# Performance work log

Measured on AMD Instinct MI355X. Metric: run time of the kernel, lower is better.

The kernel has to match this reference:

```python
import jax, jax.numpy as jnp
import numpy as np

NUM_HEADS = 8
WINDOW = 128  # num_previous_frames
EPS = 1e-5


def setup_inputs() -> dict:
    key = jax.random.key(0)
    ks = jax.random.split(key, 5)
    B, T, E = 8, 1024, 512
    x = jax.random.normal(ks[0], (B, T, E), dtype=jnp.float32)
    x_lengths = jax.random.randint(ks[1], (B,), 1, T + 1).astype(jnp.int32)
    gamma = jnp.ones((E,), dtype=jnp.float32)
    beta = jnp.zeros((E,), dtype=jnp.float32)
    sc_in = 1.0 / np.sqrt(E)
    w_in = jax.random.normal(ks[2], (3 * E, E), dtype=jnp.float32) * sc_in
    b_in = jnp.zeros((3 * E,), dtype=jnp.float32)
    w_out = jax.random.normal(ks[3], (E, E), dtype=jnp.float32) * sc_in
    b_out = jnp.zeros((E,), dtype=jnp.float32)
    return {"x": x, "x_lengths": x_lengths, "gamma": gamma, "beta": beta,
            "w_in": w_in, "b_in": b_in, "w_out": w_out, "b_out": b_out}


def _forward(x, gamma, beta, w_in, b_in, w_out, b_out):
    B, T, E = x.shape
    H = NUM_HEADS
    D = E // H
    # Timewise LayerNorm: normalize over channel dim per (batch, time)
    mu = jnp.mean(x, axis=-1, keepdims=True)
    var = jnp.mean(jnp.square(x - mu), axis=-1, keepdims=True)
    xn = (x - mu) * jax.lax.rsqrt(var + EPS) * gamma + beta
    # in-projection: qkv packed
    qkv = xn @ w_in.T + b_in  # [B,T,3E]
    q, k, v = jnp.split(qkv, 3, axis=-1)
    q = q.reshape(B, T, H, D)
    k = k.reshape(B, T, H, D)
    v = v.reshape(B, T, H, D)
    scale = 1.0 / np.sqrt(D)
    scores = jnp.einsum('bqhd,bkhd->bhqk', q * scale, k)  # [B,H,T,T]
    # banded causal mask: allow j in [i-WINDOW, i]
    i = jnp.arange(T)[:, None]
    j = jnp.arange(T)[None, :]
    allowed = (j <= i) & (j >= i - WINDOW)
    scores = jnp.where(allowed[None, None], scores, -jnp.inf)
    attn = jax.nn.softmax(scores, axis=-1)
    ctx = jnp.einsum('bhqk,bkhd->bqhd', attn, v).reshape(B, T, E)
    out = ctx @ w_out.T + b_out
    return out  # dropout is identity in eval mode


def reference(x, x_lengths, gamma, beta, w_in, b_in, w_out, b_out):
    del x_lengths  # unused by the original forward (no key_padding_mask passed)
    return _forward(x, gamma, beta, w_in, b_in, w_out, b_out)
```

## Files before the change

### kernel.cpp

```cpp
#include <hip/hip_runtime.h>
#include <stdint.h>

typedef __bf16 bf16;
typedef __bf16 bf16x4 __attribute__((ext_vector_type(4)));
typedef __bf16 bf16x8 __attribute__((ext_vector_type(8)));
typedef float f32x4 __attribute__((ext_vector_type(4)));

#define MFMA_16x16x32(a, b, c) __builtin_amdgcn_mfma_f32_16x16x32_bf16((a), (b), (c), 0, 0, 0)

__device__ __forceinline__ void gl_lds16(const bf16* g, bf16* l) {
    __builtin_amdgcn_global_load_lds(
        (const __attribute__((address_space(1))) void*)g,
        (__attribute__((address_space(3))) void*)l, 16, 0, 0);
}

__global__ __launch_bounds__(256) void prep_kernel(const float* __restrict__ x,
                                                   const float* __restrict__ gamma,
                                                   const float* __restrict__ beta,
                                                   const float* __restrict__ w_in,
                                                   const float* __restrict__ w_out,
                                                   bf16* __restrict__ xn,
                                                   bf16* __restrict__ cw_in,
                                                   bf16* __restrict__ cw_out) {
    const int bid = blockIdx.x;
    if (bid < 2048) {
        const int lane = threadIdx.x & 63;
        const int row = (bid << 2) + (threadIdx.x >> 6);
        const size_t base = (size_t)row * 512 + lane * 8;
        const float* xf = x + base;
        float4 a = *(const float4*)xf;
        float4 b = *(const float4*)(xf + 4);
        float f[8] = {a.x, a.y, a.z, a.w, b.x, b.y, b.z, b.w};
        float s = 0.f;
#pragma unroll
        for (int j = 0; j < 8; ++j) s += f[j];
#pragma unroll
        for (int off = 32; off >= 1; off >>= 1) s += __shfl_xor(s, off, 64);
        const float mu = s * (1.0f / 512.0f);
        float vs = 0.f;
#pragma unroll
        for (int j = 0; j < 8; ++j) { float d = f[j] - mu; vs += d * d; }
#pragma unroll
        for (int off = 32; off >= 1; off >>= 1) vs += __shfl_xor(vs, off, 64);
        const float rstd = rsqrtf(vs * (1.0f / 512.0f) + 1e-5f);
        float4 g0 = *(const float4*)(gamma + lane * 8);
        float4 g1 = *(const float4*)(gamma + lane * 8 + 4);
        float4 b0 = *(const float4*)(beta + lane * 8);
        float4 b1 = *(const float4*)(beta + lane * 8 + 4);
        float gg[8] = {g0.x, g0.y, g0.z, g0.w, g1.x, g1.y, g1.z, g1.w};
        float bb[8] = {b0.x, b0.y, b0.z, b0.w, b1.x, b1.y, b1.z, b1.w};
        bf16x8 o;
#pragma unroll
        for (int j = 0; j < 8; ++j)
            o[j] = (bf16)((f[j] - mu) * rstd * gg[j] + bb[j]);
        *(bf16x8*)(xn + base) = o;
    } else {
        const float* src;
        bf16* dst;
        int base;
        if (bid < 2432) { src = w_in;  dst = cw_in;  base = (bid - 2048) * 2048; }
        else            { src = w_out; dst = cw_out; base = (bid - 2432) * 2048; }
        const int i = base + threadIdx.x * 8;
        float4 a = *(const float4*)(src + i);
        float4 b = *(const float4*)(src + i + 4);
        float f[8] = {a.x, a.y, a.z, a.w, b.x, b.y, b.z, b.w};
        bf16x8 o;
#pragma unroll
        for (int j = 0; j < 8; ++j) o[j] = (bf16)f[j];
        *(bf16x8*)(dst + i) = o;
    }
}

template <int TM, typename OT>
__global__ __launch_bounds__(256) void gemm_bt(const bf16* __restrict__ A,
                                               const bf16* __restrict__ B,
                                               const float* __restrict__ bias,
                                               OT* __restrict__ C,
                                               int N, int K) {
    constexpr int MI = TM / 32;
    constexpr int NCA = TM * 8;
    __shared__ alignas(16) bf16 As[TM * 64];
    __shared__ alignas(16) bf16 Bs[128 * 64];
    const int tid = threadIdx.x;
    const int lane = tid & 63;
    const int wid = tid >> 6;
    const int wm = (wid >> 1) * (TM / 2), wn = (wid & 1) * 64;
    const int m0 = blockIdx.y * TM, n0 = blockIdx.x * 128;
    const int l15 = lane & 15, l16 = lane >> 4;

    f32x4 acc[MI][4] = {};

    const bf16* Abase = A + (size_t)m0 * K;
    const bf16* Bbase = B + (size_t)n0 * K;

    for (int k0 = 0; k0 < K; k0 += 64) {
#pragma unroll
        for (int c = tid; c < NCA; c += 256) {
            const int p = c / (TM * 4);
            const int r = (c % (TM * 4)) >> 2;
            const int ko = (c & 3) * 8 + p * 32;
            gl_lds16(Abase + (size_t)r * K + k0 + ko, &As[c * 8]);
        }
#pragma unroll
        for (int c = tid; c < 1024; c += 256) {
            const int p = c >> 9;
            const int r = (c & 511) >> 2;
            const int ko = (c & 3) * 8 + p * 32;
            gl_lds16(Bbase + (size_t)r * K + k0 + ko, &Bs[c * 8]);
        }
        __syncthreads();
#pragma unroll
        for (int h = 0; h < 2; ++h) {
            bf16x8 af[MI], bfr[4];
#pragma unroll
            for (int t = 0; t < MI; ++t)
                af[t] = *(const bf16x8*)&As[h * (TM * 32) + (wm + t * 16 + l15) * 32 + l16 * 8];
#pragma unroll
            for (int t = 0; t < 4; ++t)
                bfr[t] = *(const bf16x8*)&Bs[h * 4096 + (wn + t * 16 + l15) * 32 + l16 * 8];
#pragma unroll
            for (int i = 0; i < MI; ++i)
#pragma unroll
                for (int j = 0; j < 4; ++j)
                    acc[i][j] = MFMA_16x16x32(bfr[j], af[i], acc[i][j]);
        }
        __syncthreads();
    }

#pragma unroll
    for (int j = 0; j < 4; ++j) {
        const int colb = n0 + wn + j * 16 + (l16 << 2);
        const float4 bv = *(const float4*)(bias + colb);
#pragma unroll
        for (int i = 0; i < MI; ++i) {
            const int row = m0 + wm + i * 16 + l15;
            if constexpr (sizeof(OT) == 2) {
                bf16x4 o;
                o[0] = (bf16)(acc[i][j][0] + bv.x);
                o[1] = (bf16)(acc[i][j][1] + bv.y);
                o[2] = (bf16)(acc[i][j][2] + bv.z);
                o[3] = (bf16)(acc[i][j][3] + bv.w);
                *(bf16x4*)&C[(size_t)row * N + colb] = o;
            } else {
                float4 o;
                o.x = acc[i][j][0] + bv.x;
                o.y = acc[i][j][1] + bv.y;
                o.z = acc[i][j][2] + bv.z;
                o.w = acc[i][j][3] + bv.w;
                *(float4*)&C[(size_t)row * N + colb] = o;
            }
        }
    }
}

#define KS_STRIDE 72
#define VN_STRIDE 74
#define PW_STRIDE 72

__global__ __launch_bounds__(256) void attn_kernel(const bf16* __restrict__ qkv,
                                                   bf16* __restrict__ ctx) {
    __shared__ alignas(16) bf16 Ks[192 * KS_STRIDE];
    __shared__ alignas(16) bf16 Vn[192 * VN_STRIDE];
    __shared__ alignas(16) bf16 Pbuf[4 * 16 * PW_STRIDE];

    const int tid = threadIdx.x;
    const int lane = tid & 63, wid = tid >> 6;
    const int l15 = lane & 15, l16 = lane >> 4;
    const int bh = blockIdx.y, b = bh >> 3, h = bh & 7;
    const int q0 = blockIdx.x * 64;
    const int kv0 = (q0 > 128) ? (q0 - 128) : 0;
    const int nk = q0 + 64 - kv0;
    const size_t tokbase = (size_t)b * 1024;

    for (int c = tid; c < nk * 8; c += 256) {
        const int kk = c >> 3, dc = (c & 7) * 8;
        const bf16* src = qkv + (tokbase + kv0 + kk) * 1536 + h * 64 + dc;
        uint4 kw = *(const uint4*)(src + 512);
        *(uint4*)&Ks[kk * KS_STRIDE + dc] = kw;
        uint4 vw = *(const uint4*)(src + 1024);
        uint* vdst = (uint*)&Vn[kk * VN_STRIDE + dc];
        vdst[0] = vw.x; vdst[1] = vw.y; vdst[2] = vw.z; vdst[3] = vw.w;
    }

    const int qt0 = q0 + wid * 16;
    const bf16* qptr = qkv + (tokbase + qt0 + l15) * 1536 + h * 64;
    bf16x8 qa0 = *(const bf16x8*)(qptr + l16 * 8);
    bf16x8 qa1 = *(const bf16x8*)(qptr + 32 + l16 * 8);

    __syncthreads();

    bf16* Pw = &Pbuf[wid * 16 * PW_STRIDE];
    f32x4 of[4] = {};
    float mst[4], lst[4];
#pragma unroll
    for (int r = 0; r < 4; ++r) { mst[r] = -1e30f; lst[r] = 0.f; }

    const int ktstart = ((qt0 > 128) ? (qt0 - 128) : 0) & ~63;
    for (int kt = ktstart; kt <= qt0 + 15; kt += 64) {
        const int krel = kt - kv0;
        int kgn = ((qt0 + 15 - kt) >> 4) + 1;
        if (kgn > 4) kgn = 4;
        const int dlo = qt0 - 128 - kt;
        const int kglo = (dlo > 0) ? (dlo >> 4) : 0;

        f32x4 s[4] = {};
        __builtin_amdgcn_s_setprio(1);
#pragma unroll
        for (int kg = 0; kg < 4; ++kg) {
            if (kg >= kglo && kg < kgn) {
                const bf16* kb = &Ks[(krel + kg * 16 + l15) * KS_STRIDE + l16 * 8];
                s[kg] = MFMA_16x16x32(qa0, *(const bf16x8*)kb, s[kg]);
                s[kg] = MFMA_16x16x32(qa1, *(const bf16x8*)(kb + 32), s[kg]);
            }
        }
        __builtin_amdgcn_s_setprio(0);

#pragma unroll
        for (int r = 0; r < 4; ++r) {
            const int qa = qt0 + l16 * 4 + r;
            float v[4];
#pragma unroll
            for (int kg = 0; kg < 4; ++kg) {
                const int key = kt + kg * 16 + l15;
                const bool ok = (key <= qa) && (key >= qa - 128);
                v[kg] = ok ? s[kg][r] * 0.125f : -1e30f;
            }
            float mx = fmaxf(fmaxf(v[0], v[1]), fmaxf(v[2], v[3]));
#pragma unroll
            for (int off = 1; off < 16; off <<= 1)
                mx = fmaxf(mx, __shfl_xor(mx, off, 64));
            const float mnew = fmaxf(mst[r], mx);
            const float alpha = __expf(mst[r] - mnew);
            const float e0 = __expf(v[0] - mnew);
            const float e1 = __expf(v[1] - mnew);
            const float e2 = __expf(v[2] - mnew);
            const float e3 = __expf(v[3] - mnew);
            float rs = (e0 + e1) + (e2 + e3);
#pragma unroll
            for (int off = 1; off < 16; off <<= 1)
                rs += __shfl_xor(rs, off, 64);
            lst[r] = lst[r] * alpha + rs;
            mst[r] = mnew;
#pragma unroll
            for (int nt = 0; nt < 4; ++nt) of[nt][r] *= alpha;
            const int q = l16 * 4 + r;
            Pw[q * PW_STRIDE + l15] = (bf16)e0;
            Pw[q * PW_STRIDE + 16 + l15] = (bf16)e1;
            Pw[q * PW_STRIDE + 32 + l15] = (bf16)e2;
            Pw[q * PW_STRIDE + 48 + l15] = (bf16)e3;
        }
        __asm__ volatile("s_waitcnt lgkmcnt(0)" ::: "memory");

        const bool haveA = (kglo < 2);
        const bool haveB = (kgn > 2);
        __builtin_amdgcn_s_setprio(1);
        if (haveA) {
            bf16x8 pa = *(const bf16x8*)&Pw[l15 * PW_STRIDE + l16 * 8];
            int row[8];
#pragma unroll
            for (int j = 0; j < 8; ++j) {
                int rr = krel + l16 * 8 + j;
                row[j] = (rr < nk) ? rr : (nk - 1);
            }
#pragma unroll
            for (int nt = 0; nt < 4; ++nt) {
                bf16x8 vb;
#pragma unroll
                for (int j = 0; j < 8; ++j)
                    vb[j] = Vn[row[j] * VN_STRIDE + nt * 16 + l15];
                of[nt] = MFMA_16x16x32(pa, vb, of[nt]);
            }
        }
        if (haveB) {
            bf16x8 pa = *(const bf16x8*)&Pw[l15 * PW_STRIDE + 32 + l16 * 8];
            int row[8];
#pragma unroll
            for (int j = 0; j < 8; ++j) {
                int rr = krel + 32 + l16 * 8 + j;
                row[j] = (rr < nk) ? rr : (nk - 1);
            }
#pragma unroll
            for (int nt = 0; nt < 4; ++nt) {
                bf16x8 vb;
#pragma unroll
                for (int j = 0; j < 8; ++j)
                    vb[j] = Vn[row[j] * VN_STRIDE + nt * 16 + l15];
                of[nt] = MFMA_16x16x32(pa, vb, of[nt]);
            }
        }
        __builtin_amdgcn_s_setprio(0);
        __asm__ volatile("s_waitcnt lgkmcnt(0)" ::: "memory");
    }

    float linv[4];
#pragma unroll
    for (int r = 0; r < 4; ++r) linv[r] = 1.0f / lst[r];
    bf16* cbase = ctx + (tokbase + qt0) * 512 + h * 64;
#pragma unroll
    for (int nt = 0; nt < 4; ++nt)
#pragma unroll
        for (int r = 0; r < 4; ++r) {
            const int q = l16 * 4 + r;
            cbase[(size_t)q * 512 + nt * 16 + l15] = (bf16)(of[nt][r] * linv[r]);
        }
}

extern "C" void kernel_launch(void* const* d_in, const int* in_sizes, int n_in,
                              void* d_out, int out_size, void* d_ws, size_t ws_size,
                              hipStream_t stream) {
    const float* x     = (const float*)d_in[0];
    const float* gamma = (const float*)d_in[2];
    const float* beta  = (const float*)d_in[3];
    const float* w_in  = (const float*)d_in[4];
    const float* b_in  = (const float*)d_in[5];
    const float* w_out = (const float*)d_in[6];
    const float* b_out = (const float*)d_in[7];
    float* out = (float*)d_out;

    char* ws = (char*)d_ws;
    bf16* cw_in  = (bf16*)ws;
    bf16* cw_out = cw_in + 786432;
    bf16* xn     = (bf16*)(ws + (4u << 20));
    bf16* qkv    = (bf16*)(ws + (12u << 20));
    bf16* ctx    = xn;

    prep_kernel<<<2560, 256, 0, stream>>>(x, gamma, beta, w_in, w_out, xn, cw_in, cw_out);
    gemm_bt<128, bf16><<<dim3(12, 64), 256, 0, stream>>>(xn, cw_in, b_in, qkv, 1536, 512);
    attn_kernel<<<dim3(16, 64), 256, 0, stream>>>(qkv, ctx);
    gemm_bt<64, float><<<dim3(4, 128), 256, 0, stream>>>(ctx, cw_out, b_out, out, 512, 512);
}
```

Baseline: 145.7 us.

## Store V transposed with XOR swizzle in LDS and remap attention block order

V is now staged into shared memory transposed (head dimension as rows, key pairs packed) with an XOR swizzle. Each MFMA B operand can then be fetched with a single 16-byte LDS read instead of eight scalar 2-byte gathers. The block index is also swizzled so neighbouring workgroups are spread across batch-heads, and a trailing lgkmcnt wait is removed. The cost is a more complex staging loop and the loss of the row clamp for out-of-range keys, which relies on masked P values being zero.

```diff
diff --git a/kernel.cpp b/kernel.cpp
--- a/kernel.cpp
+++ b/kernel.cpp
@@ -154,32 +154,45 @@
 }
 
 #define KS_STRIDE 72
-#define VN_STRIDE 74
 #define PW_STRIDE 72
+#define VT_ROWB 400
 
 __global__ __launch_bounds__(256) void attn_kernel(const bf16* __restrict__ qkv,
                                                    bf16* __restrict__ ctx) {
     __shared__ alignas(16) bf16 Ks[192 * KS_STRIDE];
-    __shared__ alignas(16) bf16 Vn[192 * VN_STRIDE];
+    __shared__ alignas(16) char Vt[64 * VT_ROWB];
     __shared__ alignas(16) bf16 Pbuf[4 * 16 * PW_STRIDE];
 
     const int tid = threadIdx.x;
     const int lane = tid & 63, wid = tid >> 6;
     const int l15 = lane & 15, l16 = lane >> 4;
-    const int bh = blockIdx.y, b = bh >> 3, h = bh & 7;
-    const int q0 = blockIdx.x * 64;
+    const int bid = blockIdx.y * 16 + blockIdx.x;
+    const int swz = (bid & 7) * 128 + (bid >> 3);
+    const int bh = swz >> 4, b = bh >> 3, h = bh & 7;
+    const int q0 = (swz & 15) * 64;
     const int kv0 = (q0 > 128) ? (q0 - 128) : 0;
     const int nk = q0 + 64 - kv0;
     const size_t tokbase = (size_t)b * 1024;
 
     for (int c = tid; c < nk * 8; c += 256) {
         const int kk = c >> 3, dc = (c & 7) * 8;
-        const bf16* src = qkv + (tokbase + kv0 + kk) * 1536 + h * 64 + dc;
-        uint4 kw = *(const uint4*)(src + 512);
-        *(uint4*)&Ks[kk * KS_STRIDE + dc] = kw;
-        uint4 vw = *(const uint4*)(src + 1024);
-        uint* vdst = (uint*)&Vn[kk * VN_STRIDE + dc];
-        vdst[0] = vw.x; vdst[1] = vw.y; vdst[2] = vw.z; vdst[3] = vw.w;
+        const bf16* src = qkv + (tokbase + kv0 + kk) * 1536 + h * 64 + dc + 512;
+        *(uint4*)&Ks[kk * KS_STRIDE + dc] = *(const uint4*)src;
+    }
+    for (int c = tid; c < nk * 4; c += 256) {
+        const int kp = c >> 3, dc = (c & 7) * 8;
+        const bf16* s0 = qkv + (tokbase + kv0 + 2 * kp) * 1536 + h * 64 + dc + 1024;
+        uint4 w0 = *(const uint4*)s0;
+        uint4 w1 = *(const uint4*)(s0 + 1536);
+        const unsigned short* a0 = (const unsigned short*)&w0;
+        const unsigned short* a1 = (const unsigned short*)&w1;
+        const int u = kp >> 2, wb = (kp & 3) * 4;
+#pragma unroll
+        for (int j = 0; j < 8; ++j) {
+            const int d = dc + j;
+            *(uint*)&Vt[d * VT_ROWB + ((u ^ (d & 7)) << 4) + wb] =
+                (uint)a0[j] | ((uint)a1[j] << 16);
+        }
     }
 
     const int qt0 = q0 + wid * 16;
@@ -253,43 +266,27 @@
 
         const bool haveA = (kglo < 2);
         const bool haveB = (kgn > 2);
+        const int ub = krel >> 3;
         __builtin_amdgcn_s_setprio(1);
         if (haveA) {
             bf16x8 pa = *(const bf16x8*)&Pw[l15 * PW_STRIDE + l16 * 8];
-            int row[8];
-#pragma unroll
-            for (int j = 0; j < 8; ++j) {
-                int rr = krel + l16 * 8 + j;
-                row[j] = (rr < nk) ? rr : (nk - 1);
-            }
 #pragma unroll
             for (int nt = 0; nt < 4; ++nt) {
-                bf16x8 vb;
-#pragma unroll
-                for (int j = 0; j < 8; ++j)
-                    vb[j] = Vn[row[j] * VN_STRIDE + nt * 16 + l15];
+                const int d = nt * 16 + l15;
+                bf16x8 vb = *(const bf16x8*)&Vt[d * VT_ROWB + (((ub + l16) ^ (d & 7)) << 4)];
                 of[nt] = MFMA_16x16x32(pa, vb, of[nt]);
             }
         }
         if (haveB) {
             bf16x8 pa = *(const bf16x8*)&Pw[l15 * PW_STRIDE + 32 + l16 * 8];
-            int row[8];
-#pragma unroll
-            for (int j = 0; j < 8; ++j) {
-                int rr = krel + 32 + l16 * 8 + j;
-                row[j] = (rr < nk) ? rr : (nk - 1);
-            }
 #pragma unroll
             for (int nt = 0; nt < 4; ++nt) {
-                bf16x8 vb;
-#pragma unroll
-                for (int j = 0; j < 8; ++j)
-                    vb[j] = Vn[row[j] * VN_STRIDE + nt * 16 + l15];
+                const int d = nt * 16 + l15;
+                bf16x8 vb = *(const bf16x8*)&Vt[d * VT_ROWB + (((ub + 4 + l16) ^ (d & 7)) << 4)];
                 of[nt] = MFMA_16x16x32(pa, vb, of[nt]);
             }
         }
         __builtin_amdgcn_s_setprio(0);
-        __asm__ volatile("s_waitcnt lgkmcnt(0)" ::: "memory");
     }
 
     float linv[4];
```

Result: faster. 141.8 us (-2.7%).
